# Optimization experiments

Hardware: AMD Instinct MI355X
Metric: run time of the kernel (lower is better)

Reference implementation:

```python
import jax, jax.numpy as jnp
import numpy as np
import math

B, H, W = 8, 512, 1024
BOUNDARY_WIDTH = 4
BOUNDARY_ITERATION = 4
KERNEL_SIZE = 7
DILATION_SIZE = 6
NEG = -1e30  # geodesic border for morphological dilation (kornia border_type='geodesic')
POS = 1e30   # geodesic border for erosion
DN = ('NCHW', 'OIHW', 'NCHW')


def _gaussian_kernel():
    size, sigma = 7, 1.0
    g = np.fromfunction(
        lambda x, y: 1.0 / (2 * math.pi * sigma ** 2)
        * math.e ** (-(((x - (size - 1) / 2) ** 2 + (y - (size - 1) / 2) ** 2) / (2 * sigma ** 2))),
        (size, size))
    g = g / g.sum()
    return jnp.asarray(g, jnp.float32)[None, None]  # [1,1,7,7]


def _cross_dilate(x):
    # morphological dilation with 3x3 cross structuring element (generate_binary_structure(2,1))
    p = jnp.pad(x, ((0, 0), (0, 0), (1, 1), (1, 1)), constant_values=NEG)
    c = p[..., 1:-1, 1:-1]
    return jnp.maximum(
        jnp.maximum(jnp.maximum(c, p[..., :-2, 1:-1]), p[..., 2:, 1:-1]),
        jnp.maximum(p[..., 1:-1, :-2], p[..., 1:-1, 2:]))


def _erode3(x):
    # morphological erosion with full 3x3 ones structuring element, geodesic border
    return jax.lax.reduce_window(x, jnp.float32(POS), jax.lax.min,
                                 (1, 1, 3, 3), (1, 1, 1, 1),
                                 [(0, 0), (0, 0), (1, 1), (1, 1)])


def _conv3_sum(x):
    # 3x3 all-ones conv (first_conv), VALID on already-padded input
    k = jnp.ones((1, 1, 3, 3), x.dtype)
    return jax.lax.conv_general_dilated(x, k, (1, 1), 'VALID', dimension_numbers=DN)


def _forward(x, prediction):
    lab = prediction.astype(jnp.float32)
    # boundaries where dilated labels differ from eroded labels
    boundaries = (_cross_dilate(lab) != _erode3(lab)).astype(jnp.float32)
    out = x
    diff = BOUNDARY_WIDTH // BOUNDARY_ITERATION
    for it in range(BOUNDARY_ITERATION):
        prev = out
        r = 0 if (BOUNDARY_WIDTH == 0 or it == BOUNDARY_ITERATION - 1) else BOUNDARY_WIDTH - diff * it - 1
        eb = boundaries
        for _ in range(r):  # dilation by diamond of radius r == r cross-dilations
            eb = _cross_dilate(eb)
        mask = (eb == 0).astype(jnp.float32)  # non-boundary mask
        xm = out * mask
        xp = jnp.pad(xm, ((0, 0), (0, 0), (1, 1), (1, 1)), mode='edge')       # ReplicationPad2d(1)
        mp = jnp.pad(mask, ((0, 0), (0, 0), (1, 1), (1, 1)), mode='edge')
        y = _conv3_sum(xp)
        n = _conv3_sum(mp).astype(jnp.int32)  # .long() truncation; values are exact small ints
        n_safe = jnp.where(n == 0, 1, n).astype(y.dtype)
        avg = jnp.where(n == 0, prev, y / n_safe)
        out = jnp.where(mask == 0, avg, prev)
    # dilated gaussian smoothing: ReplicationPad2d(18) + 7x7 conv, dilation 6
    pad = DILATION_SIZE * 3
    op = jnp.pad(out, ((0, 0), (0, 0), (pad, pad), (pad, pad)), mode='edge')
    out = jax.lax.conv_general_dilated(op, _gaussian_kernel(), (1, 1), 'VALID',
                                       rhs_dilation=(DILATION_SIZE, DILATION_SIZE),
                                       dimension_numbers=DN)
    return out


def setup_inputs() -> dict:
    key = jax.random.key(0)
    k1, k2 = jax.random.split(key)
    x = jax.random.normal(k1, (B, 1, H, W), dtype=jnp.float32)
    prediction = jax.random.randint(k2, (B, 1, H, W), 0, 19, dtype=jnp.int32)
    return {"x": x, "prediction": prediction}


def reference(x, prediction):
    return _forward(x, prediction)
```

## Files before the change

### kernel.cpp

```cpp
#include <hip/hip_runtime.h>

#define B_ 8
#define H_ 512
#define W_ 1024
#define NPX (B_*H_*W_)

#define TILE 32
#define HD 4
#define RD 40
#define HB 7
#define RB 46
#define HP 8
#define RP 48

__device__ __forceinline__ int clampi(int v, int lo, int hi) {
    return v < lo ? lo : (v > hi ? hi : v);
}
__device__ __forceinline__ int imax(int a, int b) { return a > b ? a : b; }
__device__ __forceinline__ int imin(int a, int b) { return a < b ? a : b; }

__global__ __launch_bounds__(256)
void k_flags(const int* __restrict__ pred, unsigned long long* __restrict__ bmap)
{
    const int tid = threadIdx.x;
    const int idx = blockIdx.x * 256 + tid;
    const int gx   = idx & (W_ - 1);
    const int grow = idx >> 10;
    const int yi   = grow & (H_ - 1);
    const int rup  = (yi == 0)      ? grow : grow - 1;
    const int rdn  = (yi == H_ - 1) ? grow : grow + 1;

    const int c = pred[(size_t)grow * W_ + gx];
    const int u = pred[(size_t)rup  * W_ + gx];
    const int d = pred[(size_t)rdn  * W_ + gx];
    const int vmax = imax(c, imax(u, d));
    int       vmin = imin(c, imin(u, d));

    const int lane = tid & 63;
    int cL = __shfl_up(c, 1);
    int vL = __shfl_up(vmin, 1);
    int cR = __shfl_down(c, 1);
    int vR = __shfl_down(vmin, 1);
    if (lane == 0) {
        if (gx > 0) {
            cL = pred[(size_t)grow * W_ + gx - 1];
            int u2 = pred[(size_t)rup * W_ + gx - 1];
            int d2 = pred[(size_t)rdn * W_ + gx - 1];
            vL = imin(cL, imin(u2, d2));
        } else { cL = c; vL = vmin; }
    }
    if (lane == 63) {
        if (gx < W_ - 1) {
            cR = pred[(size_t)grow * W_ + gx + 1];
            int u2 = pred[(size_t)rup * W_ + gx + 1];
            int d2 = pred[(size_t)rdn * W_ + gx + 1];
            vR = imin(cR, imin(u2, d2));
        } else { cR = c; vR = vmin; }
    }
    const int mx = imax(vmax, imax(cL, cR));
    const int mn = imin(vmin, imin(vL, vR));
    const bool boundary = (mx > c) || (mn < c);
    unsigned long long bal = __ballot(boundary);
    if (lane == 0) bmap[idx >> 6] = bal;
}

__global__ __launch_bounds__(256)
void k_stage1(const float* __restrict__ xg, const int* __restrict__ predg,
              const unsigned long long* __restrict__ bmap, int use_bmap,
              float* __restrict__ outg)
{
    __shared__ int sFlag;
    __shared__ int sScratch[3200];
    __shared__ unsigned long long sB[4][RB];
    __shared__ float sA[RD * RD];
    __shared__ float sC[RD * RD];

    int*   sPred = sScratch;
    float* sHX = (float*)sScratch;
    float* sHM = (float*)sScratch + RD * RD;

    const int tid = threadIdx.x;
    const int x0 = blockIdx.x * TILE;
    const int y0 = blockIdx.y * TILE;
    const size_t plane = (size_t)H_ * W_;
    const int*   pp = predg + blockIdx.z * plane;
    const float* xp = xg    + blockIdx.z * plane;
    float*       op = outg  + blockIdx.z * plane;

    if (tid < 64) {
        bool ok = (use_bmap != 0);
        if (ok) {
            const int rlo = (y0 > 0) ? y0 - 1 : 0;
            const int rhi = (y0 + TILE < H_) ? y0 + TILE : H_ - 1;
            const int row = rlo + tid;
            if (row <= rhi) {
                const int clo = (x0 > 0) ? x0 - 1 : 0;
                const int chi = (x0 + TILE < W_) ? x0 + TILE : W_ - 1;
                const unsigned long long* rb = bmap + ((size_t)blockIdx.z * H_ + row) * (W_ / 64);
                const int w0 = clo >> 6, w1 = chi >> 6;
                for (int w = w0; w <= w1; ++w) {
                    int lo = (clo > (w << 6)) ? (clo - (w << 6)) : 0;
                    int hi = (chi < ((w << 6) + 63)) ? (chi - (w << 6)) : 63;
                    unsigned long long m = (lo == 0 && hi == 63) ? ~0ULL
                                         : ((((1ULL << (hi - lo + 1)) - 1ULL) << lo));
                    if ((rb[w] & m) != m) ok = false;
                }
            }
        }
        unsigned long long all = __ballot(ok);
        if (tid == 0) sFlag = (all == ~0ULL) ? 1 : 0;
    }
    __syncthreads();

    if (sFlag) {
        int ty = tid >> 3, tx4 = (tid & 7) * 4;
        const float4 v = *(const float4*)(xp + (size_t)(y0 + ty) * W_ + (x0 + tx4));
        *(float4*)(op + (size_t)(y0 + ty) * W_ + (x0 + tx4)) = v;
        return;
    }

    const bool leftB  = (x0 == 0), rightB = (x0 + TILE == W_);
    const bool topB   = (y0 == 0), botB   = (y0 + TILE == H_);
    const bool borderB = leftB || rightB || topB || botB;

    for (int i = tid; i < RP * RP; i += 256) {
        int ry = i / RP, rx = i - ry * RP;
        int gy = y0 - HP + ry, gx = x0 - HP + rx;
        sPred[i] = (gy >= 0 && gy < H_ && gx >= 0 && gx < W_) ? pp[(size_t)gy * W_ + gx] : -1;
    }
    for (int i = tid; i < RD * RD; i += 256) {
        int ry = i / RD, rx = i - ry * RD;
        int gy = clampi(y0 - HD + ry, 0, H_ - 1);
        int gx = clampi(x0 - HD + rx, 0, W_ - 1);
        sA[i] = xp[(size_t)gy * W_ + gx];
    }
    __syncthreads();

    {
        const int lane = tid & 63, wv = tid >> 6;
        for (int row = wv; row < RB; row += 4) {
            bool bp = false;
            if (lane < RB) {
                const int py = row + 1, px = lane + 1;
                int c = sPred[py * RP + px];
                if (c >= 0) {
                    int up = sPred[(py - 1) * RP + px];
                    int dn = sPred[(py + 1) * RP + px];
                    int lf = sPred[py * RP + px - 1];
                    int rt = sPred[py * RP + px + 1];
                    int ul = sPred[(py - 1) * RP + px - 1];
                    int ur = sPred[(py - 1) * RP + px + 1];
                    int dl = sPred[(py + 1) * RP + px - 1];
                    int dr = sPred[(py + 1) * RP + px + 1];
                    int mx = imax(imax(up, dn), imax(lf, rt));
                    int Bv = 0x7fffffff;
                    int mn = imin(imin(imin(up < 0 ? Bv : up, dn < 0 ? Bv : dn),
                                       imin(lf < 0 ? Bv : lf, rt < 0 ? Bv : rt)),
                                  imin(imin(ul < 0 ? Bv : ul, ur < 0 ? Bv : ur),
                                       imin(dl < 0 ? Bv : dl, dr < 0 ? Bv : dr)));
                    bp = (mx > c) || (mn < c);
                }
            }
            unsigned long long bal = __ballot(bp);
            if (lane == 0) sB[0][row] = bal;
        }
    }

    #pragma unroll
    for (int lvl = 1; lvl < 4; ++lvl) {
        __syncthreads();
        if (tid < RB) {
            unsigned long long c = sB[lvl - 1][tid];
            unsigned long long u = (tid > 0)      ? sB[lvl - 1][tid - 1] : 0ULL;
            unsigned long long d = (tid < RB - 1) ? sB[lvl - 1][tid + 1] : 0ULL;
            sB[lvl][tid] = c | (c << 1) | (c >> 1) | u | d;
        }
    }
    __syncthreads();

    if (borderB) {
        const bool act = tid < 4 * RB;
        unsigned long long val = 0; int lvl = 0, row = 0;
        if (act) {
            lvl = tid / RB; row = tid - lvl * RB;
            int srcRow = clampi(row, topB ? HB : 0, botB ? (RB - 1 - HB) : RB - 1);
            val = sB[lvl][srcRow];
            if (leftB) {
                unsigned long long b = (val >> HB) & 1ULL;
                unsigned long long lo = (1ULL << HB) - 1;
                val = (val & ~lo) | (b ? lo : 0ULL);
            }
            if (rightB) {
                const int jb = RB - 1 - HB;
                unsigned long long b = (val >> jb) & 1ULL;
                unsigned long long keep = (1ULL << (jb + 1)) - 1;
                unsigned long long hi = (((1ULL << RB) - 1) & ~keep);
                val = (val & keep) | (b ? hi : 0ULL);
            }
        }
        __syncthreads();
        if (act) sB[lvl][row] = val;
    }
    __syncthreads();

    float* cur = sA;
    float* nxt = sC;
    #pragma unroll
    for (int it = 0; it < 4; ++it) {
        const int r = 3 - it;
        const unsigned long long* br = sB[r];

        for (int i = tid; i < RD * RD; i += 256) {
            int ry = i / RD, rx = i - ry * RD;
            unsigned long long row = br[ry + (HB - HD)];
            int rxm = rx > 0 ? rx - 1 : 0;
            int rxp = rx < RD - 1 ? rx + 1 : RD - 1;
            float m0 = ((row >> (rx + 2)) & 1ULL) ? 0.f : 1.f;
            float m1 = ((row >> (rx + 3)) & 1ULL) ? 0.f : 1.f;
            float m2 = ((row >> (rx + 4)) & 1ULL) ? 0.f : 1.f;
            float a0 = cur[ry * RD + rxm];
            float a1 = cur[ry * RD + rx];
            float a2 = cur[ry * RD + rxp];
            sHX[i] = m0 * a0 + m1 * a1 + m2 * a2;
            sHM[i] = m0 + m1 + m2;
        }
        __syncthreads();

        for (int i = tid; i < 38 * 38; i += 256) {
            int q = i / 38;
            int ry = 1 + q, rx = 1 + (i - q * 38);
            int idx = ry * RD + rx;
            float n = sHM[idx - RD] + sHM[idx] + sHM[idx + RD];
            float y = sHX[idx - RD] + sHX[idx] + sHX[idx + RD];
            float c = cur[idx];
            unsigned long long row = br[ry + (HB - HD)];
            bool masked = ((row >> (rx + 3)) & 1ULL) != 0ULL;
            float avg = y * __builtin_amdgcn_rcpf(n);
            nxt[idx] = (masked && n > 0.5f) ? avg : c;
        }
        __syncthreads();

        if (borderB) {
            for (int i = tid; i < RD * RD; i += 256) {
                int ry = i / RD, rx = i - ry * RD;
                int ryc = clampi(ry, topB ? HD : 0, botB ? (RD - 1 - HD) : RD - 1);
                int rxc = clampi(rx, leftB ? HD : 0, rightB ? (RD - 1 - HD) : RD - 1);
                if (ryc != ry || rxc != rx) nxt[i] = nxt[ryc * RD + rxc];
            }
        }
        __syncthreads();
        float* t = cur; cur = nxt; nxt = t;
    }

    for (int i = tid; i < TILE * TILE; i += 256) {
        int ty = i >> 5, tx = i & 31;
        op[(size_t)(y0 + ty) * W_ + (x0 + tx)] = cur[(ty + HD) * RD + (tx + HD)];
    }
}

#define GW0 0.39905027965f
#define GW1 0.24203622800f
#define GW2 0.05400558260f
#define GW3 0.00443304810f

__global__ __launch_bounds__(256)
void gaussH(const float* __restrict__ in, float* __restrict__ out)
{
    const int tid = threadIdx.x;
    const float* rp = in  + (size_t)blockIdx.x * W_;
    float*       wp = out + (size_t)blockIdx.x * W_;
    const int gx0 = tid * 4;

    float4 o;
    if (tid >= 5 && tid <= 250) {
        const float4* vp = (const float4*)(rp + gx0 - 20);
        float4 fm5 = vp[0], fm4 = vp[1], fm3 = vp[2], fm2 = vp[3], fm1 = vp[4];
        float4 f0 = vp[5], f1 = vp[6], f2 = vp[7], f3 = vp[8], f4 = vp[9], f5 = vp[10];
        o.x = GW0 * f0.x + GW1 * (fm2.z + f1.z) + GW2 * (fm3.x + f3.x) + GW3 * (fm5.z + f4.z);
        o.y = GW0 * f0.y + GW1 * (fm2.w + f1.w) + GW2 * (fm3.y + f3.y) + GW3 * (fm5.w + f4.w);
        o.z = GW0 * f0.z + GW1 * (fm1.x + f2.x) + GW2 * (fm3.z + f3.z) + GW3 * (fm4.x + f5.x);
        o.w = GW0 * f0.w + GW1 * (fm1.y + f2.y) + GW2 * (fm3.w + f3.w) + GW3 * (fm4.y + f5.y);
    } else {
        float r[4];
        #pragma unroll
        for (int j = 0; j < 4; ++j) {
            int gx = gx0 + j;
            r[j] = GW3 * (rp[clampi(gx - 18, 0, W_ - 1)] + rp[clampi(gx + 18, 0, W_ - 1)])
                 + GW2 * (rp[clampi(gx - 12, 0, W_ - 1)] + rp[clampi(gx + 12, 0, W_ - 1)])
                 + GW1 * (rp[clampi(gx - 6,  0, W_ - 1)] + rp[clampi(gx + 6,  0, W_ - 1)])
                 + GW0 *  rp[gx];
        }
        o.x = r[0]; o.y = r[1]; o.z = r[2]; o.w = r[3];
    }
    *(float4*)(wp + gx0) = o;
}

__global__ __launch_bounds__(256)
void gaussV(const float* __restrict__ in, float* __restrict__ out)
{
    const int tid = threadIdx.x;
    const int y   = blockIdx.x & (H_ - 1);
    const int img = blockIdx.x >> 9;
    const float* pl = in  + (size_t)img * H_ * W_;
    float*       wp = out + (size_t)blockIdx.x * W_;
    const int gx0 = tid * 4;

    const float* r0 = pl + (size_t)clampi(y - 18, 0, H_ - 1) * W_ + gx0;
    const float* r1 = pl + (size_t)clampi(y - 12, 0, H_ - 1) * W_ + gx0;
    const float* r2 = pl + (size_t)clampi(y - 6,  0, H_ - 1) * W_ + gx0;
    const float* r3 = pl + (size_t)y * W_ + gx0;
    const float* r4 = pl + (size_t)clampi(y + 6,  0, H_ - 1) * W_ + gx0;
    const float* r5 = pl + (size_t)clampi(y + 12, 0, H_ - 1) * W_ + gx0;
    const float* r6 = pl + (size_t)clampi(y + 18, 0, H_ - 1) * W_ + gx0;

    float4 a0 = *(const float4*)r0, a1 = *(const float4*)r1, a2 = *(const float4*)r2;
    float4 a3 = *(const float4*)r3, a4 = *(const float4*)r4, a5 = *(const float4*)r5;
    float4 a6 = *(const float4*)r6;

    float4 o;
    o.x = GW3 * (a0.x + a6.x) + GW2 * (a1.x + a5.x) + GW1 * (a2.x + a4.x) + GW0 * a3.x;
    o.y = GW3 * (a0.y + a6.y) + GW2 * (a1.y + a5.y) + GW1 * (a2.y + a4.y) + GW0 * a3.y;
    o.z = GW3 * (a0.z + a6.z) + GW2 * (a1.z + a5.z) + GW1 * (a2.z + a4.z) + GW0 * a3.z;
    o.w = GW3 * (a0.w + a6.w) + GW2 * (a1.w + a5.w) + GW1 * (a2.w + a4.w) + GW0 * a3.w;
    *(float4*)(wp + gx0) = o;
}

#define GTW 64
#define GTH 64
#define GHALO 18
#define GRH (GTH + 2*GHALO)

__global__ __launch_bounds__(256)
void bsws_stage2_tiled(const float* __restrict__ ing, float* __restrict__ outg)
{
    __shared__ float sH[GRH][GTW];
    const int tid = threadIdx.x;
    const int x0 = blockIdx.x * GTW;
    const int y0 = blockIdx.y * GTH;
    const size_t plane = (size_t)H_ * W_;
    const float* ip = ing  + blockIdx.z * plane;
    float*       op = outg + blockIdx.z * plane;

    for (int i = tid; i < GRH * GTW; i += 256) {
        int row = i >> 6, col = i & 63;
        int gy = clampi(y0 - GHALO + row, 0, H_ - 1);
        const float* rowp = ip + (size_t)gy * W_;
        int gx = x0 + col;
        float acc = GW3 * (rowp[clampi(gx - 18, 0, W_ - 1)] + rowp[clampi(gx + 18, 0, W_ - 1)])
                  + GW2 * (rowp[clampi(gx - 12, 0, W_ - 1)] + rowp[clampi(gx + 12, 0, W_ - 1)])
                  + GW1 * (rowp[clampi(gx - 6,  0, W_ - 1)] + rowp[clampi(gx + 6,  0, W_ - 1)])
                  + GW0 *  rowp[gx];
        sH[row][col] = acc;
    }
    __syncthreads();
    for (int i = tid; i < GTH * GTW; i += 256) {
        int ty = i >> 6, tx = i & 63;
        float acc = GW3 * (sH[ty][tx]      + sH[ty + 36][tx])
                  + GW2 * (sH[ty + 6][tx]  + sH[ty + 30][tx])
                  + GW1 * (sH[ty + 12][tx] + sH[ty + 24][tx])
                  + GW0 *  sH[ty + 18][tx];
        op[(size_t)(y0 + ty) * W_ + (x0 + tx)] = acc;
    }
}

extern "C" void kernel_launch(void* const* d_in, const int* in_sizes, int n_in,
                              void* d_out, int out_size, void* d_ws, size_t ws_size,
                              hipStream_t stream) {
    const float* x    = (const float*)d_in[0];
    const int*   pred = (const int*)d_in[1];
    float*       out  = (float*)d_out;
    float*       mid  = (float*)d_ws;

    const size_t plane_bytes = (size_t)NPX * 4;
    const size_t bmap_bytes  = (size_t)NPX / 8;

    if (ws_size >= 2 * plane_bytes + bmap_bytes) {
        float* midH = mid + NPX;
        unsigned long long* bmap = (unsigned long long*)((char*)d_ws + 2 * plane_bytes);
        k_flags<<<NPX / 256, 256, 0, stream>>>(pred, bmap);
        k_stage1<<<dim3(W_ / TILE, H_ / TILE, B_), dim3(256), 0, stream>>>(x, pred, bmap, 1, mid);
        gaussH<<<B_ * H_, 256, 0, stream>>>(mid, midH);
        gaussV<<<B_ * H_, 256, 0, stream>>>(midH, out);
    } else if (ws_size >= 2 * plane_bytes) {
        float* midH = mid + NPX;
        k_stage1<<<dim3(W_ / TILE, H_ / TILE, B_), dim3(256), 0, stream>>>(x, pred, nullptr, 0, mid);
        gaussH<<<B_ * H_, 256, 0, stream>>>(mid, midH);
        gaussV<<<B_ * H_, 256, 0, stream>>>(midH, out);
    } else {
        k_stage1<<<dim3(W_ / TILE, H_ / TILE, B_), dim3(256), 0, stream>>>(x, pred, nullptr, 0, mid);
        bsws_stage2_tiled<<<dim3(W_ / GTW, H_ / GTH, B_), dim3(256), 0, stream>>>(mid, out);
    }
}
```

Before: 129.8 us.

## Fuse boundary-flag pass into stage1 and skip writing clean tiles via per-tile flags

Drops the separate k_flags kernel and its bitmap. Stage1 now checks each tile itself from a 36x36 prediction patch in shared memory. Clean tiles write a per-tile flag byte instead of copying x into mid, and gaussH reads x directly for rows with no dirty tiles, picking from mid or x per tap otherwise. This saves one launch, a full pass over pred and the copy traffic for clean tiles. The cost is extra flag lookups in gaussH and the slow clamped path for mixed rows.

```diff
diff --git a/kernel.cpp b/kernel.cpp
--- a/kernel.cpp
+++ b/kernel.cpp
@@ -12,6 +12,7 @@
 #define RB 46
 #define HP 8
 #define RP 48
+#define TP 36
 
 __device__ __forceinline__ int clampi(int v, int lo, int hi) {
     return v < lo ? lo : (v > hi ? hi : v);
@@ -20,60 +21,14 @@
 __device__ __forceinline__ int imin(int a, int b) { return a < b ? a : b; }
 
 __global__ __launch_bounds__(256)
-void k_flags(const int* __restrict__ pred, unsigned long long* __restrict__ bmap)
+void k_stage1(const float* __restrict__ xg, const int* __restrict__ predg,
+              float* __restrict__ midg, unsigned char* __restrict__ flags)
 {
-    const int tid = threadIdx.x;
-    const int idx = blockIdx.x * 256 + tid;
-    const int gx   = idx & (W_ - 1);
-    const int grow = idx >> 10;
-    const int yi   = grow & (H_ - 1);
-    const int rup  = (yi == 0)      ? grow : grow - 1;
-    const int rdn  = (yi == H_ - 1) ? grow : grow + 1;
-
-    const int c = pred[(size_t)grow * W_ + gx];
-    const int u = pred[(size_t)rup  * W_ + gx];
-    const int d = pred[(size_t)rdn  * W_ + gx];
-    const int vmax = imax(c, imax(u, d));
-    int       vmin = imin(c, imin(u, d));
-
-    const int lane = tid & 63;
-    int cL = __shfl_up(c, 1);
-    int vL = __shfl_up(vmin, 1);
-    int cR = __shfl_down(c, 1);
-    int vR = __shfl_down(vmin, 1);
-    if (lane == 0) {
-        if (gx > 0) {
-            cL = pred[(size_t)grow * W_ + gx - 1];
-            int u2 = pred[(size_t)rup * W_ + gx - 1];
-            int d2 = pred[(size_t)rdn * W_ + gx - 1];
-            vL = imin(cL, imin(u2, d2));
-        } else { cL = c; vL = vmin; }
-    }
-    if (lane == 63) {
-        if (gx < W_ - 1) {
-            cR = pred[(size_t)grow * W_ + gx + 1];
-            int u2 = pred[(size_t)rup * W_ + gx + 1];
-            int d2 = pred[(size_t)rdn * W_ + gx + 1];
-            vR = imin(cR, imin(u2, d2));
-        } else { cR = c; vR = vmin; }
-    }
-    const int mx = imax(vmax, imax(cL, cR));
-    const int mn = imin(vmin, imin(vL, vR));
-    const bool boundary = (mx > c) || (mn < c);
-    unsigned long long bal = __ballot(boundary);
-    if (lane == 0) bmap[idx >> 6] = bal;
-}
-
-__global__ __launch_bounds__(256)
-void k_stage1(const float* __restrict__ xg, const int* __restrict__ predg,
-              const unsigned long long* __restrict__ bmap, int use_bmap,
-              float* __restrict__ outg)
-{
-    __shared__ int sFlag;
     __shared__ int sScratch[3200];
     __shared__ unsigned long long sB[4][RB];
     __shared__ float sA[RD * RD];
     __shared__ float sC[RD * RD];
+    __shared__ int sV[4];
 
     int*   sPred = sScratch;
     float* sHX = (float*)sScratch;
@@ -85,37 +40,56 @@
     const size_t plane = (size_t)H_ * W_;
     const int*   pp = predg + blockIdx.z * plane;
     const float* xp = xg    + blockIdx.z * plane;
-    float*       op = outg  + blockIdx.z * plane;
-
-    if (tid < 64) {
-        bool ok = (use_bmap != 0);
-        if (ok) {
-            const int rlo = (y0 > 0) ? y0 - 1 : 0;
-            const int rhi = (y0 + TILE < H_) ? y0 + TILE : H_ - 1;
-            const int row = rlo + tid;
-            if (row <= rhi) {
-                const int clo = (x0 > 0) ? x0 - 1 : 0;
-                const int chi = (x0 + TILE < W_) ? x0 + TILE : W_ - 1;
-                const unsigned long long* rb = bmap + ((size_t)blockIdx.z * H_ + row) * (W_ / 64);
-                const int w0 = clo >> 6, w1 = chi >> 6;
-                for (int w = w0; w <= w1; ++w) {
-                    int lo = (clo > (w << 6)) ? (clo - (w << 6)) : 0;
-                    int hi = (chi < ((w << 6) + 63)) ? (chi - (w << 6)) : 63;
-                    unsigned long long m = (lo == 0 && hi == 63) ? ~0ULL
-                                         : ((((1ULL << (hi - lo + 1)) - 1ULL) << lo));
-                    if ((rb[w] & m) != m) ok = false;
-                }
-            }
-        }
-        unsigned long long all = __ballot(ok);
-        if (tid == 0) sFlag = (all == ~0ULL) ? 1 : 0;
-    }
-    __syncthreads();
-
-    if (sFlag) {
-        int ty = tid >> 3, tx4 = (tid & 7) * 4;
-        const float4 v = *(const float4*)(xp + (size_t)(y0 + ty) * W_ + (x0 + tx4));
-        *(float4*)(op + (size_t)(y0 + ty) * W_ + (x0 + tx4)) = v;
+    float*       op = midg  + blockIdx.z * plane;
+
+    for (int i = tid; i < TP * TP; i += 256) {
+        int ry = i / TP, rx = i - ry * TP;
+        int gy = y0 - 2 + ry, gx = x0 - 2 + rx;
+        sPred[i] = (gy >= 0 && gy < H_ && gx >= 0 && gx < W_) ? pp[(size_t)gy * W_ + gx] : -1;
+    }
+    __syncthreads();
+
+    const int lane = tid & 63, wv = tid >> 6;
+    unsigned long long acc = 0ULL;
+    for (int r = wv; r < TILE + 2; r += 4) {
+        bool viol = false;
+        if (lane < TILE + 2) {
+            int gy = y0 - 1 + r, gx = x0 - 1 + lane;
+            if (gy >= 0 && gy < H_ && gx >= 0 && gx < W_) {
+                const int py = r + 1, px = lane + 1;
+                int c  = sPred[py * TP + px];
+                int up = sPred[(py - 1) * TP + px];
+                int dn = sPred[(py + 1) * TP + px];
+                int lf = sPred[py * TP + px - 1];
+                int rt = sPred[py * TP + px + 1];
+                int ul = sPred[(py - 1) * TP + px - 1];
+                int ur = sPred[(py - 1) * TP + px + 1];
+                int dl = sPred[(py + 1) * TP + px - 1];
+                int dr = sPred[(py + 1) * TP + px + 1];
+                int mx = imax(imax(up, dn), imax(lf, rt));
+                int Bv = 0x7fffffff;
+                int mn = imin(imin(imin(up < 0 ? Bv : up, dn < 0 ? Bv : dn),
+                                   imin(lf < 0 ? Bv : lf, rt < 0 ? Bv : rt)),
+                              imin(imin(ul < 0 ? Bv : ul, ur < 0 ? Bv : ur),
+                                   imin(dl < 0 ? Bv : dl, dr < 0 ? Bv : dr)));
+                viol = !((mx > c) || (mn < c));
+            }
+        }
+        acc |= __ballot(viol);
+    }
+    if (lane == 0) sV[wv] = (acc != 0ULL) ? 1 : 0;
+    __syncthreads();
+    const bool dirty = (sV[0] | sV[1] | sV[2] | sV[3]) != 0;
+
+    const int tileId = (((blockIdx.z << 4) + blockIdx.y) << 5) + blockIdx.x;
+    if (!dirty) {
+        if (flags) {
+            if (tid == 0) flags[tileId] = 0;
+        } else {
+            int ty = tid >> 3, tx4 = (tid & 7) * 4;
+            const float4 v = *(const float4*)(xp + (size_t)(y0 + ty) * W_ + (x0 + tx4));
+            *(float4*)(op + (size_t)(y0 + ty) * W_ + (x0 + tx4)) = v;
+        }
         return;
     }
 
@@ -123,6 +97,7 @@
     const bool topB   = (y0 == 0), botB   = (y0 + TILE == H_);
     const bool borderB = leftB || rightB || topB || botB;
 
+    __syncthreads();
     for (int i = tid; i < RP * RP; i += 256) {
         int ry = i / RP, rx = i - ry * RP;
         int gy = y0 - HP + ry, gx = x0 - HP + rx;
@@ -137,7 +112,6 @@
     __syncthreads();
 
     {
-        const int lane = tid & 63, wv = tid >> 6;
         for (int row = wv; row < RB; row += 4) {
             bool bp = false;
             if (lane < RB) {
@@ -256,6 +230,7 @@
         int ty = i >> 5, tx = i & 31;
         op[(size_t)(y0 + ty) * W_ + (x0 + tx)] = cur[(ty + HD) * RD + (tx + HD)];
     }
+    if (flags && tid == 0) flags[tileId] = 1;
 }
 
 #define GW0 0.39905027965f
@@ -264,31 +239,63 @@
 #define GW3 0.00443304810f
 
 __global__ __launch_bounds__(256)
-void gaussH(const float* __restrict__ in, float* __restrict__ out)
+void gaussH(const float* __restrict__ x, const float* __restrict__ mid,
+            const unsigned char* __restrict__ flags, float* __restrict__ out)
 {
+    __shared__ int sDirty;
     const int tid = threadIdx.x;
-    const float* rp = in  + (size_t)blockIdx.x * W_;
-    float*       wp = out + (size_t)blockIdx.x * W_;
+    const int grow = blockIdx.x;
+    const int img = grow >> 9, y = grow & (H_ - 1);
+    const int fbase = (((img << 4) + (y >> 5)) << 5);
+
+    if (tid == 0) sDirty = 0;
+    __syncthreads();
+    if (tid < 64) {
+        int f = (tid < 32) ? (int)flags[fbase + tid] : 0;
+        bool any = __any(f != 0);
+        if (tid == 0 && any) sDirty = 1;
+    }
+    __syncthreads();
+
+    const float* rp = x   + (size_t)grow * W_;
+    float*       wp = out + (size_t)grow * W_;
     const int gx0 = tid * 4;
-
     float4 o;
-    if (tid >= 5 && tid <= 250) {
-        const float4* vp = (const float4*)(rp + gx0 - 20);
-        float4 fm5 = vp[0], fm4 = vp[1], fm3 = vp[2], fm2 = vp[3], fm1 = vp[4];
-        float4 f0 = vp[5], f1 = vp[6], f2 = vp[7], f3 = vp[8], f4 = vp[9], f5 = vp[10];
-        o.x = GW0 * f0.x + GW1 * (fm2.z + f1.z) + GW2 * (fm3.x + f3.x) + GW3 * (fm5.z + f4.z);
-        o.y = GW0 * f0.y + GW1 * (fm2.w + f1.w) + GW2 * (fm3.y + f3.y) + GW3 * (fm5.w + f4.w);
-        o.z = GW0 * f0.z + GW1 * (fm1.x + f2.x) + GW2 * (fm3.z + f3.z) + GW3 * (fm4.x + f5.x);
-        o.w = GW0 * f0.w + GW1 * (fm1.y + f2.y) + GW2 * (fm3.w + f3.w) + GW3 * (fm4.y + f5.y);
+
+    if (!sDirty) {
+        if (tid >= 5 && tid <= 250) {
+            const float4* vp = (const float4*)(rp + gx0 - 20);
+            float4 fm5 = vp[0], fm4 = vp[1], fm3 = vp[2], fm2 = vp[3], fm1 = vp[4];
+            float4 f0 = vp[5], f1 = vp[6], f2 = vp[7], f3 = vp[8], f4 = vp[9], f5 = vp[10];
+            o.x = GW0 * f0.x + GW1 * (fm2.z + f1.z) + GW2 * (fm3.x + f3.x) + GW3 * (fm5.z + f4.z);
+            o.y = GW0 * f0.y + GW1 * (fm2.w + f1.w) + GW2 * (fm3.y + f3.y) + GW3 * (fm5.w + f4.w);
+            o.z = GW0 * f0.z + GW1 * (fm1.x + f2.x) + GW2 * (fm3.z + f3.z) + GW3 * (fm4.x + f5.x);
+            o.w = GW0 * f0.w + GW1 * (fm1.y + f2.y) + GW2 * (fm3.w + f3.w) + GW3 * (fm4.y + f5.y);
+        } else {
+            float r[4];
+            #pragma unroll
+            for (int j = 0; j < 4; ++j) {
+                int gx = gx0 + j;
+                r[j] = GW3 * (rp[clampi(gx - 18, 0, W_ - 1)] + rp[clampi(gx + 18, 0, W_ - 1)])
+                     + GW2 * (rp[clampi(gx - 12, 0, W_ - 1)] + rp[clampi(gx + 12, 0, W_ - 1)])
+                     + GW1 * (rp[clampi(gx - 6,  0, W_ - 1)] + rp[clampi(gx + 6,  0, W_ - 1)])
+                     + GW0 *  rp[gx];
+            }
+            o.x = r[0]; o.y = r[1]; o.z = r[2]; o.w = r[3];
+        }
     } else {
+        const float* rm = mid + (size_t)grow * W_;
         float r[4];
         #pragma unroll
         for (int j = 0; j < 4; ++j) {
             int gx = gx0 + j;
-            r[j] = GW3 * (rp[clampi(gx - 18, 0, W_ - 1)] + rp[clampi(gx + 18, 0, W_ - 1)])
-                 + GW2 * (rp[clampi(gx - 12, 0, W_ - 1)] + rp[clampi(gx + 12, 0, W_ - 1)])
-                 + GW1 * (rp[clampi(gx - 6,  0, W_ - 1)] + rp[clampi(gx + 6,  0, W_ - 1)])
-                 + GW0 *  rp[gx];
+            float t[7];
+            #pragma unroll
+            for (int k = 0; k < 7; ++k) {
+                int q = clampi(gx + (k - 3) * 6, 0, W_ - 1);
+                t[k] = flags[fbase + (q >> 5)] ? rm[q] : rp[q];
+            }
+            r[j] = GW3 * (t[0] + t[6]) + GW2 * (t[1] + t[5]) + GW1 * (t[2] + t[4]) + GW0 * t[3];
         }
         o.x = r[0]; o.y = r[1]; o.z = r[2]; o.w = r[3];
     }
@@ -372,22 +379,16 @@
     float*       mid  = (float*)d_ws;
 
     const size_t plane_bytes = (size_t)NPX * 4;
-    const size_t bmap_bytes  = (size_t)NPX / 8;
-
-    if (ws_size >= 2 * plane_bytes + bmap_bytes) {
+    const dim3 g1(W_ / TILE, H_ / TILE, B_);
+
+    if (ws_size >= 2 * plane_bytes + 4096) {
         float* midH = mid + NPX;
-        unsigned long long* bmap = (unsigned long long*)((char*)d_ws + 2 * plane_bytes);
-        k_flags<<<NPX / 256, 256, 0, stream>>>(pred, bmap);
-        k_stage1<<<dim3(W_ / TILE, H_ / TILE, B_), dim3(256), 0, stream>>>(x, pred, bmap, 1, mid);
-        gaussH<<<B_ * H_, 256, 0, stream>>>(mid, midH);
-        gaussV<<<B_ * H_, 256, 0, stream>>>(midH, out);
-    } else if (ws_size >= 2 * plane_bytes) {
-        float* midH = mid + NPX;
-        k_stage1<<<dim3(W_ / TILE, H_ / TILE, B_), dim3(256), 0, stream>>>(x, pred, nullptr, 0, mid);
-        gaussH<<<B_ * H_, 256, 0, stream>>>(mid, midH);
+        unsigned char* flags = (unsigned char*)d_ws + 2 * plane_bytes;
+        k_stage1<<<g1, 256, 0, stream>>>(x, pred, mid, flags);
+        gaussH<<<B_ * H_, 256, 0, stream>>>(x, mid, flags, midH);
         gaussV<<<B_ * H_, 256, 0, stream>>>(midH, out);
     } else {
-        k_stage1<<<dim3(W_ / TILE, H_ / TILE, B_), dim3(256), 0, stream>>>(x, pred, nullptr, 0, mid);
+        k_stage1<<<g1, 256, 0, stream>>>(x, pred, mid, nullptr);
         bsws_stage2_tiled<<<dim3(W_ / GTW, H_ / GTH, B_), dim3(256), 0, stream>>>(mid, out);
     }
 }
```

Result: no change. 129.0 us (-0.7%).
